# Optimization experiments

Measured on AMD Instinct MI355X. Metric: run time of the kernel, lower is better.

## Reference

```python
import jax, jax.numpy as jnp
import numpy as np

K_CLUSTERS = 512
N_ITERS = 10  # fixed Lloyd iterations (torch_kmeans uses max_iter with tol; fixed count keeps it jit-friendly)


def setup_inputs() -> dict:
    key = jax.random.key(0)
    x = jax.random.normal(key, (4, 8192, 256), dtype=jnp.float32)  # (B, N, D)
    return {"x": x}


def _sq_dists(x, centers):
    # x: (B,N,D), centers: (B,K,D) -> squared Euclidean distances (B,N,K)
    xc = jnp.einsum('bnd,bkd->bnk', x, centers)
    x2 = jnp.sum(x * x, axis=-1, keepdims=True)          # (B,N,1)
    c2 = jnp.sum(centers * centers, axis=-1)[:, None, :]  # (B,1,K)
    return x2 - 2.0 * xc + c2


def _kmeans(x, k=K_CLUSTERS, iters=N_ITERS):
    # deterministic init: first k points of each batch as initial centroids
    centers0 = x[:, :k, :]  # (B,K,D)

    def step(centers, _):
        labels = jnp.argmin(_sq_dists(x, centers), axis=-1)          # (B,N)
        onehot = jax.nn.one_hot(labels, k, dtype=x.dtype)            # (B,N,K)
        sums = jnp.einsum('bnk,bnd->bkd', onehot, x)                 # (B,K,D)
        counts = jnp.sum(onehot, axis=1)                             # (B,K)
        new_centers = jnp.where(
            counts[..., None] > 0,
            sums / jnp.maximum(counts, 1.0)[..., None],
            centers,  # keep empty clusters' previous centroid
        )
        return new_centers, None

    centers, _ = jax.lax.scan(step, centers0, None, length=iters)
    labels = jnp.argmin(_sq_dists(x, centers), axis=-1)
    return labels, centers


def reference(x):
    labels, centers = _kmeans(x)
    return labels, centers
```

## Files before the change

### kernel.cpp

```cpp
#include <hip/hip_runtime.h>
#include <math.h>

#define BB 4
#define NN 8192
#define DD 256
#define KK 512
#define NITERS 10

#define TAU 0.02f
#define NCH 128

typedef _Float16 f16;
typedef f16   f16x8 __attribute__((ext_vector_type(8)));
typedef float f32x4 __attribute__((ext_vector_type(4)));

__global__ __launch_bounds__(256) void init_centers_k(const float* __restrict__ x,
                                                      float* __restrict__ centers,
                                                      f16* __restrict__ chh,
                                                      f16* __restrict__ chl,
                                                      float* __restrict__ c2) {
    __shared__ float sq[256];
    int bk = blockIdx.x;
    int b  = bk >> 9;
    int k  = bk & 511;
    int t  = threadIdx.x;
    size_t idx = (size_t)bk * DD + t;
    float v = x[((size_t)b * NN + k) * DD + t];
    centers[idx] = v;
    f16 h = (f16)v;
    chh[idx] = h;
    chl[idx] = (f16)(v - (float)h);
    sq[t] = v * v;
    __syncthreads();
    for (int s = 128; s > 0; s >>= 1) {
        if (t < s) sq[t] += sq[t + s];
        __syncthreads();
    }
    if (t == 0) c2[bk] = sq[0];
}

__global__ __launch_bounds__(256) void rowsumsq_k(const float* __restrict__ rows,
                                                  float* __restrict__ out, int nrows) {
    int r = blockIdx.x * 256 + threadIdx.x;
    if (r >= nrows) return;
    const float* p = rows + (size_t)r * DD;
    float total = 0.f;
    #pragma unroll
    for (int h = 0; h < 2; ++h) {
        float a[8];
        #pragma unroll
        for (int j = 0; j < 8; ++j) a[j] = 0.f;
        for (int i = 0; i < 128; i += 8) {
            #pragma unroll
            for (int j = 0; j < 8; ++j) {
                float v  = p[h * 128 + i + j];
                float sq = __fmul_rn(v, v);
                a[j] = __fadd_rn(a[j], sq);
            }
        }
        float s = __fadd_rn(__fadd_rn(__fadd_rn(a[0], a[1]), __fadd_rn(a[2], a[3])),
                            __fadd_rn(__fadd_rn(a[4], a[5]), __fadd_rn(a[6], a[7])));
        total = __fadd_rn(total, s);
    }
    out[r] = total;
}

__global__ __launch_bounds__(256, 2) void assign_k(
    const float* __restrict__ x,
    const f16* __restrict__ chh, const f16* __restrict__ chl,
    const float* __restrict__ x2g, const float* __restrict__ c2g,
    int* __restrict__ labels, int* __restrict__ flagslot, int* __restrict__ flaglist)
{
    __shared__ f16 xlh[64 * 256];
    __shared__ f16 xll[64 * 256];
    __shared__ float rv1s[4][64];
    __shared__ float rv2s[4][64];
    __shared__ int   rk1s[4][64];

    const int tid  = threadIdx.x;
    const int wid  = tid >> 6;
    const int lane = tid & 63;
    const int l15  = lane & 15;
    const int lg   = lane >> 4;
    const int b    = blockIdx.x >> 7;
    const int m0   = (blockIdx.x & 127) * 64;

    const float* xb = x + (size_t)(b * NN + m0) * DD;

    #pragma unroll
    for (int i = 0; i < 8; ++i) {
        int lin = tid + i * 256;
        int row = lin >> 5, g = lin & 31;
        const float* p = xb + row * DD + g * 8;
        float4 a  = *(const float4*)p;
        float4 bq = *(const float4*)(p + 4);
        float vf[8] = {a.x, a.y, a.z, a.w, bq.x, bq.y, bq.z, bq.w};
        f16x8 hv, lv;
        #pragma unroll
        for (int j = 0; j < 8; ++j) {
            f16 h = (f16)vf[j];
            hv[j] = h;
            lv[j] = (f16)(vf[j] - (float)h);
        }
        int si = row * 256 + ((g ^ (row & 7)) << 3);
        *(f16x8*)&xlh[si] = hv;
        *(f16x8*)&xll[si] = lv;
    }
    __syncthreads();

    const f16* bhb = chh + ((size_t)b * KK + wid * 128) * DD;
    const f16* blb = chl + ((size_t)b * KK + wid * 128) * DD;

    f32x4 acc[4][8];
    #pragma unroll
    for (int mi = 0; mi < 4; ++mi)
        #pragma unroll
        for (int ki = 0; ki < 8; ++ki)
            acc[mi][ki] = (f32x4){0.f, 0.f, 0.f, 0.f};

    for (int d0 = 0; d0 < DD; d0 += 32) {
        f16x8 ah[4], al[4];
        #pragma unroll
        for (int mi = 0; mi < 4; ++mi) {
            int row = mi * 16 + l15;
            int g   = (d0 >> 3) + lg;
            int si  = row * 256 + ((g ^ (row & 7)) << 3);
            ah[mi] = *(const f16x8*)&xlh[si];
            al[mi] = *(const f16x8*)&xll[si];
        }
        #pragma unroll
        for (int ki = 0; ki < 8; ++ki) {
            size_t off = (size_t)(ki * 16 + l15) * DD + d0 + lg * 8;
            f16x8 bh = *(const f16x8*)(bhb + off);
            f16x8 bl = *(const f16x8*)(blb + off);
            #pragma unroll
            for (int mi = 0; mi < 4; ++mi) {
                acc[mi][ki] = __builtin_amdgcn_mfma_f32_16x16x32_f16(ah[mi], bh, acc[mi][ki], 0, 0, 0);
                acc[mi][ki] = __builtin_amdgcn_mfma_f32_16x16x32_f16(ah[mi], bl, acc[mi][ki], 0, 0, 0);
                acc[mi][ki] = __builtin_amdgcn_mfma_f32_16x16x32_f16(al[mi], bh, acc[mi][ki], 0, 0, 0);
            }
        }
    }

    float c2v[8];
    #pragma unroll
    for (int ki = 0; ki < 8; ++ki)
        c2v[ki] = c2g[b * KK + wid * 128 + ki * 16 + l15];

    #pragma unroll
    for (int mi = 0; mi < 4; ++mi) {
        #pragma unroll
        for (int r = 0; r < 4; ++r) {
            int p = mi * 16 + lg * 4 + r;
            float x2p = x2g[b * NN + m0 + p];
            float v1 = __builtin_inff(), v2 = __builtin_inff();
            int   k1 = 0x7fffffff;
            #pragma unroll
            for (int ki = 0; ki < 8; ++ki) {
                float s    = acc[mi][ki][r];
                float cand = __fadd_rn(__fsub_rn(x2p, __fmul_rn(2.0f, s)), c2v[ki]);
                int   kidx = wid * 128 + ki * 16 + l15;
                if (cand < v1 || (cand == v1 && kidx < k1)) { v2 = v1; v1 = cand; k1 = kidx; }
                else if (cand < v2) v2 = cand;
            }
            #pragma unroll
            for (int off = 1; off < 16; off <<= 1) {
                float ov1 = __shfl_xor(v1, off, 64);
                int   ok1 = __shfl_xor(k1, off, 64);
                float ov2 = __shfl_xor(v2, off, 64);
                if (ov1 < v1 || (ov1 == v1 && ok1 < k1)) { v2 = fminf(v1, ov2); v1 = ov1; k1 = ok1; }
                else v2 = fminf(v2, ov1);
            }
            if (l15 == 0) { rv1s[wid][p] = v1; rv2s[wid][p] = v2; rk1s[wid][p] = k1; }
        }
    }
    __syncthreads();
    if (tid < 64) {
        float v1 = rv1s[0][tid], v2 = rv2s[0][tid];
        int   k1 = rk1s[0][tid];
        #pragma unroll
        for (int w = 1; w < 4; ++w) {
            float ov1 = rv1s[w][tid], ov2 = rv2s[w][tid];
            int   ok1 = rk1s[w][tid];
            if (ov1 < v1 || (ov1 == v1 && ok1 < k1)) { v2 = fminf(v1, ov2); v1 = ov1; k1 = ok1; }
            else v2 = fminf(v2, ov1);
        }
        int g = b * NN + m0 + tid;
        labels[g] = k1;
        if (v2 - v1 < TAU) {
            int pos = atomicAdd(flagslot, 1);
            flaglist[pos] = g;
        }
    }
}

__global__ __launch_bounds__(256) void refine_k(const float* __restrict__ x,
                                                const float* __restrict__ centers,
                                                const int* __restrict__ flagslot,
                                                const int* __restrict__ flaglist,
                                                int* __restrict__ labels) {
    __shared__ float  xsr[DD];
    __shared__ double sv[256];
    __shared__ int    si[256];
    const int t = threadIdx.x;
    const int cnt = flagslot[0];
    for (int idx = blockIdx.x; idx < cnt; idx += gridDim.x) {
        const int g = flaglist[idx];
        const int b = g >> 13;
        __syncthreads();
        xsr[t] = x[(size_t)g * DD + t];
        __syncthreads();
        const float* cbase = centers + (size_t)b * KK * DD;
        double bestv = 1e300; int bestk = 0x7fffffff;
        #pragma unroll
        for (int h = 0; h < 2; ++h) {
            int k = t + h * 256;
            const float* cr = cbase + (size_t)k * DD;
            double a0 = 0, a1 = 0, a2 = 0, a3 = 0;
            for (int d = 0; d < DD; d += 4) {
                float4 cv = *(const float4*)(cr + d);
                double f0 = (double)xsr[d + 0] - (double)cv.x;
                double f1 = (double)xsr[d + 1] - (double)cv.y;
                double f2 = (double)xsr[d + 2] - (double)cv.z;
                double f3 = (double)xsr[d + 3] - (double)cv.w;
                a0 += f0 * f0; a1 += f1 * f1; a2 += f2 * f2; a3 += f3 * f3;
            }
            double dist = (a0 + a1) + (a2 + a3);
            if (dist < bestv || (dist == bestv && k < bestk)) { bestv = dist; bestk = k; }
        }
        sv[t] = bestv; si[t] = bestk;
        __syncthreads();
        for (int s = 128; s > 0; s >>= 1) {
            if (t < s) {
                if (sv[t + s] < sv[t] || (sv[t + s] == sv[t] && si[t + s] < si[t])) {
                    sv[t] = sv[t + s]; si[t] = si[t + s];
                }
            }
            __syncthreads();
        }
        if (t == 0) labels[g] = si[0];
    }
}

__global__ __launch_bounds__(64) void chunk_hist_k(const int* __restrict__ labels,
                                                   int* __restrict__ chunkhist) {
    __shared__ int h[KK];
    const int bc = blockIdx.x;
    const int b  = bc >> 7;
    const int c  = bc & (NCH - 1);
    const int t  = threadIdx.x;
    for (int k = t; k < KK; k += 64) h[k] = 0;
    __syncthreads();
    int l = labels[b * NN + c * 64 + t];
    atomicAdd(&h[l], 1);
    __syncthreads();
    int* ch = chunkhist + (size_t)bc * KK;
    for (int k = t; k < KK; k += 64) ch[k] = h[k];
}

__global__ __launch_bounds__(64) void scan_cols_k(int* __restrict__ chunkhist,
                                                  int* __restrict__ counts) {
    const int bq = blockIdx.x;
    const int b  = bq >> 3;
    const int k  = (bq & 7) * 64 + threadIdx.x;
    int* ch = chunkhist + (size_t)b * NCH * KK;
    int run = 0;
    for (int c0 = 0; c0 < NCH; c0 += 16) {
        int v[16];
        #pragma unroll
        for (int j = 0; j < 16; ++j) v[j] = ch[(size_t)(c0 + j) * KK + k];
        #pragma unroll
        for (int j = 0; j < 16; ++j) {
            ch[(size_t)(c0 + j) * KK + k] = run;
            run += v[j];
        }
    }
    counts[b * KK + k] = run;
}

__global__ __launch_bounds__(512) void scan_offsets_k(const int* __restrict__ counts,
                                                      int* __restrict__ offsets) {
    __shared__ int s[KK];
    const int b = blockIdx.x;
    const int k = threadIdx.x;
    int run = counts[b * KK + k];
    s[k] = run;
    __syncthreads();
    for (int off = 1; off < KK; off <<= 1) {
        int v = (k >= off) ? s[k - off] : 0;
        __syncthreads();
        s[k] += v;
        __syncthreads();
    }
    offsets[b * KK + k] = s[k] - run;
}

__global__ __launch_bounds__(64) void scatter_k(const int* __restrict__ labels,
                                                const int* __restrict__ chunkhist,
                                                const int* __restrict__ offsets,
                                                int* __restrict__ idxlist) {
    const int bc = blockIdx.x;
    const int b  = bc >> 7;
    const int c  = bc & (NCH - 1);
    const int t  = threadIdx.x;
    const int n  = c * 64 + t;
    const int l  = labels[b * NN + n];
    int rank = 0;
    for (int j = 0; j < 64; ++j) {
        int lj = __shfl(l, j, 64);
        rank += (lj == l && j < t) ? 1 : 0;
    }
    int base = offsets[b * KK + l] + chunkhist[(size_t)bc * KK + l];
    idxlist[b * NN + base + rank] = n;
}

__global__ __launch_bounds__(1024) void centers_update_k(const float* __restrict__ x,
                                                         float* __restrict__ centers,
                                                         f16* __restrict__ chh,
                                                         f16* __restrict__ chl,
                                                         float* __restrict__ c2,
                                                         const int* __restrict__ counts,
                                                         const int* __restrict__ offsets,
                                                         const int* __restrict__ idxlist) {
    __shared__ float part[16][DD];
    __shared__ float sq[256];
    const int bk   = blockIdx.x;
    const int b    = bk >> 9;
    const int tid  = threadIdx.x;
    const int w    = tid >> 6;
    const int lane = tid & 63;
    const int cnt = counts[bk];
    if (cnt == 0) return;
    const int* il = idxlist + b * NN + offsets[bk];
    const float* xb = x + (size_t)b * NN * DD;
    float4 acc = {0.f, 0.f, 0.f, 0.f};
    #pragma unroll 4
    for (int j = w; j < cnt; j += 16) {
        int n = il[j];
        float4 v = *(const float4*)(xb + (size_t)n * DD + lane * 4);
        acc.x = __fadd_rn(acc.x, v.x);
        acc.y = __fadd_rn(acc.y, v.y);
        acc.z = __fadd_rn(acc.z, v.z);
        acc.w = __fadd_rn(acc.w, v.w);
    }
    *(float4*)&part[w][lane * 4] = acc;
    __syncthreads();
    float val = 0.f;
    if (tid < DD) {
        float s = 0.f;
        #pragma unroll
        for (int w2 = 0; w2 < 16; ++w2) s = __fadd_rn(s, part[w2][tid]);
        val = s / (float)cnt;
        size_t idx = (size_t)bk * DD + tid;
        centers[idx] = val;
        f16 h = (f16)val;
        chh[idx] = h;
        chl[idx] = (f16)(val - (float)h);
    }
    if (tid < 256) sq[tid] = val * val;
    __syncthreads();
    for (int s = 128; s > 0; s >>= 1) {
        if (tid < s) sq[tid] += sq[tid + s];
        __syncthreads();
    }
    if (tid == 0) c2[bk] = sq[0];
}

__global__ __launch_bounds__(256) void out_k(const int* __restrict__ labels,
                                             const float* __restrict__ centers,
                                             float* __restrict__ out) {
    size_t i = (size_t)blockIdx.x * 256 + threadIdx.x;
    if (i < (size_t)BB * NN) out[i] = (float)labels[i];
    else                     out[i] = centers[i - (size_t)BB * NN];
}

extern "C" void kernel_launch(void* const* d_in, const int* in_sizes, int n_in,
                              void* d_out, int out_size, void* d_ws, size_t ws_size,
                              hipStream_t stream) {
    const float* x = (const float*)d_in[0];
    float* out = (float*)d_out;
    float* ws  = (float*)d_ws;

    float* centers  = ws;
    float* c2       = centers + (size_t)BB * KK * DD;
    float* x2       = c2 + BB * KK;
    int*   labels   = (int*)(x2 + BB * NN);
    int*   flagcnt  = labels + BB * NN;
    int*   flaglist = flagcnt + 64;
    int*   counts   = flaglist + BB * NN;
    int*   offsets  = counts + BB * KK;
    int*   idxlist  = offsets + BB * KK;
    int*   chunkhist= idxlist + BB * NN;
    f16*   chh      = (f16*)(chunkhist + (size_t)BB * NCH * KK);
    f16*   chl      = chh + (size_t)BB * KK * DD;

    hipMemsetAsync(flagcnt, 0, 64 * sizeof(int), stream);

    init_centers_k<<<BB * KK, 256, 0, stream>>>(x, centers, chh, chl, c2);
    rowsumsq_k<<<(BB * NN + 255) / 256, 256, 0, stream>>>(x, x2, BB * NN);

    for (int it = 0; it < NITERS; ++it) {
        assign_k<<<BB * (NN / 64), 256, 0, stream>>>(x, chh, chl, x2, c2,
                                                     labels, flagcnt + it, flaglist);
        refine_k<<<512, 256, 0, stream>>>(x, centers, flagcnt + it, flaglist, labels);
        chunk_hist_k<<<BB * NCH, 64, 0, stream>>>(labels, chunkhist);
        scan_cols_k<<<BB * 8, 64, 0, stream>>>(chunkhist, counts);
        scan_offsets_k<<<BB, 512, 0, stream>>>(counts, offsets);
        scatter_k<<<BB * NCH, 64, 0, stream>>>(labels, chunkhist, offsets, idxlist);
        centers_update_k<<<BB * KK, 1024, 0, stream>>>(x, centers, chh, chl, c2,
                                                       counts, offsets, idxlist);
    }

    assign_k<<<BB * (NN / 64), 256, 0, stream>>>(x, chh, chl, x2, c2,
                                                 labels, flagcnt + NITERS, flaglist);
    refine_k<<<512, 256, 0, stream>>>(x, centers, flagcnt + NITERS, flaglist, labels);

    out_k<<<(int)(((size_t)BB * NN + (size_t)BB * KK * DD + 255) / 256), 256, 0, stream>>>(
        labels, centers, out);
}
```

Measured before the change: 1.103 ms.

## Split assign GEMM into two passes with double-buffered center loads; merge scan kernels

The assign kernel now processes the 512 centers in two passes of 256, which halves the accumulator register footprint per pass. Within each pass, the next d-slice of center fragments is prefetched into alternating register buffers while the current slice runs through MFMA. This is meant to hide global-load latency and relieve register pressure, at the cost of reloading the x tile fragments from LDS twice and running the reduction over 8 partials. Separately, the column scan and offset scan are fused into a single kernel with 4 blocks, saving one launch per iteration but reducing parallelism in the column scan.

```diff
diff --git a/kernel.cpp b/kernel.cpp
--- a/kernel.cpp
+++ b/kernel.cpp
@@ -73,9 +73,9 @@
 {
     __shared__ f16 xlh[64 * 256];
     __shared__ f16 xll[64 * 256];
-    __shared__ float rv1s[4][64];
-    __shared__ float rv2s[4][64];
-    __shared__ int   rk1s[4][64];
+    __shared__ float rv1s[8][64];
+    __shared__ float rv2s[8][64];
+    __shared__ int   rk1s[8][64];
 
     const int tid  = threadIdx.x;
     const int wid  = tid >> 6;
@@ -108,70 +108,113 @@
     }
     __syncthreads();
 
-    const f16* bhb = chh + ((size_t)b * KK + wid * 128) * DD;
-    const f16* blb = chl + ((size_t)b * KK + wid * 128) * DD;
-
-    f32x4 acc[4][8];
     #pragma unroll
-    for (int mi = 0; mi < 4; ++mi)
-        #pragma unroll
-        for (int ki = 0; ki < 8; ++ki)
-            acc[mi][ki] = (f32x4){0.f, 0.f, 0.f, 0.f};
-
-    for (int d0 = 0; d0 < DD; d0 += 32) {
+    for (int pass = 0; pass < 2; ++pass) {
+        const f16* bhb = chh + ((size_t)b * KK + pass * 256 + wid * 64) * DD;
+        const f16* blb = chl + ((size_t)b * KK + pass * 256 + wid * 64) * DD;
+
+        f32x4 acc[4][4];
+        #pragma unroll
+        for (int mi = 0; mi < 4; ++mi)
+            #pragma unroll
+            for (int ki = 0; ki < 4; ++ki)
+                acc[mi][ki] = (f32x4){0.f, 0.f, 0.f, 0.f};
+
         f16x8 ah[4], al[4];
-        #pragma unroll
-        for (int mi = 0; mi < 4; ++mi) {
-            int row = mi * 16 + l15;
-            int g   = (d0 >> 3) + lg;
-            int si  = row * 256 + ((g ^ (row & 7)) << 3);
-            ah[mi] = *(const f16x8*)&xlh[si];
-            al[mi] = *(const f16x8*)&xll[si];
-        }
-        #pragma unroll
-        for (int ki = 0; ki < 8; ++ki) {
-            size_t off = (size_t)(ki * 16 + l15) * DD + d0 + lg * 8;
-            f16x8 bh = *(const f16x8*)(bhb + off);
-            f16x8 bl = *(const f16x8*)(blb + off);
+        f16x8 bhA[4], blA[4], bhB[4], blB[4];
+
+        #pragma unroll
+        for (int ki = 0; ki < 4; ++ki) {
+            size_t off = (size_t)(ki * 16 + l15) * DD + lg * 8;
+            bhA[ki] = *(const f16x8*)(bhb + off);
+            blA[ki] = *(const f16x8*)(blb + off);
+        }
+
+        #pragma unroll
+        for (int s = 0; s < 8; ++s) {
+            const int d0 = s * 32;
+            if (s < 7) {
+                const int dn = d0 + 32;
+                if ((s & 1) == 0) {
+                    #pragma unroll
+                    for (int ki = 0; ki < 4; ++ki) {
+                        size_t off = (size_t)(ki * 16 + l15) * DD + dn + lg * 8;
+                        bhB[ki] = *(const f16x8*)(bhb + off);
+                        blB[ki] = *(const f16x8*)(blb + off);
+                    }
+                } else {
+                    #pragma unroll
+                    for (int ki = 0; ki < 4; ++ki) {
+                        size_t off = (size_t)(ki * 16 + l15) * DD + dn + lg * 8;
+                        bhA[ki] = *(const f16x8*)(bhb + off);
+                        blA[ki] = *(const f16x8*)(blb + off);
+                    }
+                }
+            }
             #pragma unroll
             for (int mi = 0; mi < 4; ++mi) {
-                acc[mi][ki] = __builtin_amdgcn_mfma_f32_16x16x32_f16(ah[mi], bh, acc[mi][ki], 0, 0, 0);
-                acc[mi][ki] = __builtin_amdgcn_mfma_f32_16x16x32_f16(ah[mi], bl, acc[mi][ki], 0, 0, 0);
-                acc[mi][ki] = __builtin_amdgcn_mfma_f32_16x16x32_f16(al[mi], bh, acc[mi][ki], 0, 0, 0);
-            }
-        }
-    }
-
-    float c2v[8];
-    #pragma unroll
-    for (int ki = 0; ki < 8; ++ki)
-        c2v[ki] = c2g[b * KK + wid * 128 + ki * 16 + l15];
-
-    #pragma unroll
-    for (int mi = 0; mi < 4; ++mi) {
-        #pragma unroll
-        for (int r = 0; r < 4; ++r) {
-            int p = mi * 16 + lg * 4 + r;
-            float x2p = x2g[b * NN + m0 + p];
-            float v1 = __builtin_inff(), v2 = __builtin_inff();
-            int   k1 = 0x7fffffff;
+                int row = mi * 16 + l15;
+                int g   = (d0 >> 3) + lg;
+                int si  = row * 256 + ((g ^ (row & 7)) << 3);
+                ah[mi] = *(const f16x8*)&xlh[si];
+                al[mi] = *(const f16x8*)&xll[si];
+            }
+            if ((s & 1) == 0) {
+                #pragma unroll
+                for (int ki = 0; ki < 4; ++ki)
+                    #pragma unroll
+                    for (int mi = 0; mi < 4; ++mi) {
+                        acc[mi][ki] = __builtin_amdgcn_mfma_f32_16x16x32_f16(ah[mi], bhA[ki], acc[mi][ki], 0, 0, 0);
+                        acc[mi][ki] = __builtin_amdgcn_mfma_f32_16x16x32_f16(ah[mi], blA[ki], acc[mi][ki], 0, 0, 0);
+                        acc[mi][ki] = __builtin_amdgcn_mfma_f32_16x16x32_f16(al[mi], bhA[ki], acc[mi][ki], 0, 0, 0);
+                    }
+            } else {
+                #pragma unroll
+                for (int ki = 0; ki < 4; ++ki)
+                    #pragma unroll
+                    for (int mi = 0; mi < 4; ++mi) {
+                        acc[mi][ki] = __builtin_amdgcn_mfma_f32_16x16x32_f16(ah[mi], bhB[ki], acc[mi][ki], 0, 0, 0);
+                        acc[mi][ki] = __builtin_amdgcn_mfma_f32_16x16x32_f16(ah[mi], blB[ki], acc[mi][ki], 0, 0, 0);
+                        acc[mi][ki] = __builtin_amdgcn_mfma_f32_16x16x32_f16(al[mi], bhB[ki], acc[mi][ki], 0, 0, 0);
+                    }
+            }
+        }
+
+        float c2v[4];
+        #pragma unroll
+        for (int ki = 0; ki < 4; ++ki)
+            c2v[ki] = c2g[b * KK + pass * 256 + wid * 64 + ki * 16 + l15];
+
+        #pragma unroll
+        for (int mi = 0; mi < 4; ++mi) {
             #pragma unroll
-            for (int ki = 0; ki < 8; ++ki) {
-                float s    = acc[mi][ki][r];
-                float cand = __fadd_rn(__fsub_rn(x2p, __fmul_rn(2.0f, s)), c2v[ki]);
-                int   kidx = wid * 128 + ki * 16 + l15;
-                if (cand < v1 || (cand == v1 && kidx < k1)) { v2 = v1; v1 = cand; k1 = kidx; }
-                else if (cand < v2) v2 = cand;
-            }
-            #pragma unroll
-            for (int off = 1; off < 16; off <<= 1) {
-                float ov1 = __shfl_xor(v1, off, 64);
-                int   ok1 = __shfl_xor(k1, off, 64);
-                float ov2 = __shfl_xor(v2, off, 64);
-                if (ov1 < v1 || (ov1 == v1 && ok1 < k1)) { v2 = fminf(v1, ov2); v1 = ov1; k1 = ok1; }
-                else v2 = fminf(v2, ov1);
-            }
-            if (l15 == 0) { rv1s[wid][p] = v1; rv2s[wid][p] = v2; rk1s[wid][p] = k1; }
+            for (int r = 0; r < 4; ++r) {
+                int p = mi * 16 + lg * 4 + r;
+                float x2p = x2g[b * NN + m0 + p];
+                float v1 = __builtin_inff(), v2 = __builtin_inff();
+                int   k1 = 0x7fffffff;
+                #pragma unroll
+                for (int ki = 0; ki < 4; ++ki) {
+                    float sdot = acc[mi][ki][r];
+                    float cand = __fadd_rn(__fsub_rn(x2p, __fmul_rn(2.0f, sdot)), c2v[ki]);
+                    int   kidx = pass * 256 + wid * 64 + ki * 16 + l15;
+                    if (cand < v1 || (cand == v1 && kidx < k1)) { v2 = v1; v1 = cand; k1 = kidx; }
+                    else if (cand < v2) v2 = cand;
+                }
+                #pragma unroll
+                for (int off = 1; off < 16; off <<= 1) {
+                    float ov1 = __shfl_xor(v1, off, 64);
+                    int   ok1 = __shfl_xor(k1, off, 64);
+                    float ov2 = __shfl_xor(v2, off, 64);
+                    if (ov1 < v1 || (ov1 == v1 && ok1 < k1)) { v2 = fminf(v1, ov2); v1 = ov1; k1 = ok1; }
+                    else v2 = fminf(v2, ov1);
+                }
+                if (l15 == 0) {
+                    rv1s[wid * 2 + pass][p] = v1;
+                    rv2s[wid * 2 + pass][p] = v2;
+                    rk1s[wid * 2 + pass][p] = k1;
+                }
+            }
         }
     }
     __syncthreads();
@@ -179,7 +222,7 @@
         float v1 = rv1s[0][tid], v2 = rv2s[0][tid];
         int   k1 = rk1s[0][tid];
         #pragma unroll
-        for (int w = 1; w < 4; ++w) {
+        for (int w = 1; w < 8; ++w) {
             float ov1 = rv1s[w][tid], ov2 = rv2s[w][tid];
             int   ok1 = rk1s[w][tid];
             if (ov1 < v1 || (ov1 == v1 && ok1 < k1)) { v2 = fminf(v1, ov2); v1 = ov1; k1 = ok1; }
@@ -258,11 +301,12 @@
     for (int k = t; k < KK; k += 64) ch[k] = h[k];
 }
 
-__global__ __launch_bounds__(64) void scan_cols_k(int* __restrict__ chunkhist,
-                                                  int* __restrict__ counts) {
-    const int bq = blockIdx.x;
-    const int b  = bq >> 3;
-    const int k  = (bq & 7) * 64 + threadIdx.x;
+__global__ __launch_bounds__(512) void scan_k(int* __restrict__ chunkhist,
+                                              int* __restrict__ counts,
+                                              int* __restrict__ offsets) {
+    __shared__ int s[KK];
+    const int b = blockIdx.x;
+    const int k = threadIdx.x;
     int* ch = chunkhist + (size_t)b * NCH * KK;
     int run = 0;
     for (int c0 = 0; c0 < NCH; c0 += 16) {
@@ -276,14 +320,6 @@
         }
     }
     counts[b * KK + k] = run;
-}
-
-__global__ __launch_bounds__(512) void scan_offsets_k(const int* __restrict__ counts,
-                                                      int* __restrict__ offsets) {
-    __shared__ int s[KK];
-    const int b = blockIdx.x;
-    const int k = threadIdx.x;
-    int run = counts[b * KK + k];
     s[k] = run;
     __syncthreads();
     for (int off = 1; off < KK; off <<= 1) {
@@ -404,8 +440,7 @@
                                                      labels, flagcnt + it, flaglist);
         refine_k<<<512, 256, 0, stream>>>(x, centers, flagcnt + it, flaglist, labels);
         chunk_hist_k<<<BB * NCH, 64, 0, stream>>>(labels, chunkhist);
-        scan_cols_k<<<BB * 8, 64, 0, stream>>>(chunkhist, counts);
-        scan_offsets_k<<<BB, 512, 0, stream>>>(counts, offsets);
+        scan_k<<<BB, 512, 0, stream>>>(chunkhist, counts, offsets);
         scatter_k<<<BB * NCH, 64, 0, stream>>>(labels, chunkhist, offsets, idxlist);
         centers_update_k<<<BB * KK, 1024, 0, stream>>>(x, centers, chh, chl, c2,
                                                        counts, offsets, idxlist);
```

After: 1.205 ms. +9.2%, slower.

## Precompute x low-half fp16 once and merge column and offset scans

Applied to the files above, without the earlier changes.

A new kernel computes the fp16 residual (low part) of x once before the iterations. assign_k then reads that residual straight from global memory inside the MFMA loop instead of storing it in LDS, which halves its shared memory footprint. The chunk histogram is transposed to a [k][chunk] layout so a single scan kernel can do the per-cluster column scan and the cross-cluster offset scan, saving a launch per iteration. The cost is direct global reads of the A-operand low half during the inner loop, which may stall, plus extra workspace for the residual array.

```diff
diff --git a/kernel.cpp b/kernel.cpp
--- a/kernel.cpp
+++ b/kernel.cpp
@@ -39,6 +39,21 @@
     if (t == 0) c2[bk] = sq[0];
 }
 
+__global__ __launch_bounds__(256) void xsplit_k(const float* __restrict__ x,
+                                                f16* __restrict__ xl) {
+    size_t i = ((size_t)blockIdx.x * 256 + threadIdx.x) * 8;
+    float4 a  = *(const float4*)(x + i);
+    float4 bq = *(const float4*)(x + i + 4);
+    float vf[8] = {a.x, a.y, a.z, a.w, bq.x, bq.y, bq.z, bq.w};
+    f16x8 lv;
+    #pragma unroll
+    for (int j = 0; j < 8; ++j) {
+        f16 h = (f16)vf[j];
+        lv[j] = (f16)(vf[j] - (float)h);
+    }
+    *(f16x8*)(xl + i) = lv;
+}
+
 __global__ __launch_bounds__(256) void rowsumsq_k(const float* __restrict__ rows,
                                                   float* __restrict__ out, int nrows) {
     int r = blockIdx.x * 256 + threadIdx.x;
@@ -66,13 +81,12 @@
 }
 
 __global__ __launch_bounds__(256, 2) void assign_k(
-    const float* __restrict__ x,
+    const float* __restrict__ x, const f16* __restrict__ xl,
     const f16* __restrict__ chh, const f16* __restrict__ chl,
     const float* __restrict__ x2g, const float* __restrict__ c2g,
     int* __restrict__ labels, int* __restrict__ flagslot, int* __restrict__ flaglist)
 {
     __shared__ f16 xlh[64 * 256];
-    __shared__ f16 xll[64 * 256];
     __shared__ float rv1s[4][64];
     __shared__ float rv2s[4][64];
     __shared__ int   rk1s[4][64];
@@ -85,7 +99,8 @@
     const int b    = blockIdx.x >> 7;
     const int m0   = (blockIdx.x & 127) * 64;
 
-    const float* xb = x + (size_t)(b * NN + m0) * DD;
+    const float* xb  = x  + (size_t)(b * NN + m0) * DD;
+    const f16*   xlb = xl + (size_t)(b * NN + m0) * DD;
 
     #pragma unroll
     for (int i = 0; i < 8; ++i) {
@@ -95,16 +110,11 @@
         float4 a  = *(const float4*)p;
         float4 bq = *(const float4*)(p + 4);
         float vf[8] = {a.x, a.y, a.z, a.w, bq.x, bq.y, bq.z, bq.w};
-        f16x8 hv, lv;
-        #pragma unroll
-        for (int j = 0; j < 8; ++j) {
-            f16 h = (f16)vf[j];
-            hv[j] = h;
-            lv[j] = (f16)(vf[j] - (float)h);
-        }
+        f16x8 hv;
+        #pragma unroll
+        for (int j = 0; j < 8; ++j) hv[j] = (f16)vf[j];
         int si = row * 256 + ((g ^ (row & 7)) << 3);
         *(f16x8*)&xlh[si] = hv;
-        *(f16x8*)&xll[si] = lv;
     }
     __syncthreads();
 
@@ -126,8 +136,10 @@
             int g   = (d0 >> 3) + lg;
             int si  = row * 256 + ((g ^ (row & 7)) << 3);
             ah[mi] = *(const f16x8*)&xlh[si];
-            al[mi] = *(const f16x8*)&xll[si];
-        }
+        }
+        #pragma unroll
+        for (int mi = 0; mi < 4; ++mi)
+            al[mi] = *(const f16x8*)(xlb + (size_t)(mi * 16 + l15) * DD + d0 + lg * 8);
         #pragma unroll
         for (int ki = 0; ki < 8; ++ki) {
             size_t off = (size_t)(ki * 16 + l15) * DD + d0 + lg * 8;
@@ -254,36 +266,29 @@
     int l = labels[b * NN + c * 64 + t];
     atomicAdd(&h[l], 1);
     __syncthreads();
-    int* ch = chunkhist + (size_t)bc * KK;
-    for (int k = t; k < KK; k += 64) ch[k] = h[k];
-}
-
-__global__ __launch_bounds__(64) void scan_cols_k(int* __restrict__ chunkhist,
-                                                  int* __restrict__ counts) {
-    const int bq = blockIdx.x;
-    const int b  = bq >> 3;
-    const int k  = (bq & 7) * 64 + threadIdx.x;
-    int* ch = chunkhist + (size_t)b * NCH * KK;
+    for (int k = t; k < KK; k += 64)
+        chunkhist[((size_t)b * KK + k) * NCH + c] = h[k];
+}
+
+__global__ __launch_bounds__(512) void scan_k(int* __restrict__ chunkhist,
+                                              int* __restrict__ counts,
+                                              int* __restrict__ offsets) {
+    __shared__ int s[KK];
+    const int b = blockIdx.x;
+    const int k = threadIdx.x;
+    int* ch = chunkhist + ((size_t)b * KK + k) * NCH;
     int run = 0;
     for (int c0 = 0; c0 < NCH; c0 += 16) {
         int v[16];
         #pragma unroll
-        for (int j = 0; j < 16; ++j) v[j] = ch[(size_t)(c0 + j) * KK + k];
+        for (int j = 0; j < 16; ++j) v[j] = ch[c0 + j];
         #pragma unroll
         for (int j = 0; j < 16; ++j) {
-            ch[(size_t)(c0 + j) * KK + k] = run;
+            ch[c0 + j] = run;
             run += v[j];
         }
     }
     counts[b * KK + k] = run;
-}
-
-__global__ __launch_bounds__(512) void scan_offsets_k(const int* __restrict__ counts,
-                                                      int* __restrict__ offsets) {
-    __shared__ int s[KK];
-    const int b = blockIdx.x;
-    const int k = threadIdx.x;
-    int run = counts[b * KK + k];
     s[k] = run;
     __syncthreads();
     for (int off = 1; off < KK; off <<= 1) {
@@ -310,7 +315,7 @@
         int lj = __shfl(l, j, 64);
         rank += (lj == l && j < t) ? 1 : 0;
     }
-    int base = offsets[b * KK + l] + chunkhist[(size_t)bc * KK + l];
+    int base = offsets[b * KK + l] + chunkhist[((size_t)b * KK + l) * NCH + c];
     idxlist[b * NN + base + rank] = n;
 }
 
@@ -393,25 +398,26 @@
     int*   chunkhist= idxlist + BB * NN;
     f16*   chh      = (f16*)(chunkhist + (size_t)BB * NCH * KK);
     f16*   chl      = chh + (size_t)BB * KK * DD;
+    f16*   xl16     = chl + (size_t)BB * KK * DD;
 
     hipMemsetAsync(flagcnt, 0, 64 * sizeof(int), stream);
 
     init_centers_k<<<BB * KK, 256, 0, stream>>>(x, centers, chh, chl, c2);
+    xsplit_k<<<(int)((size_t)BB * NN * DD / 8 / 256), 256, 0, stream>>>(x, xl16);
     rowsumsq_k<<<(BB * NN + 255) / 256, 256, 0, stream>>>(x, x2, BB * NN);
 
     for (int it = 0; it < NITERS; ++it) {
-        assign_k<<<BB * (NN / 64), 256, 0, stream>>>(x, chh, chl, x2, c2,
+        assign_k<<<BB * (NN / 64), 256, 0, stream>>>(x, xl16, chh, chl, x2, c2,
                                                      labels, flagcnt + it, flaglist);
         refine_k<<<512, 256, 0, stream>>>(x, centers, flagcnt + it, flaglist, labels);
         chunk_hist_k<<<BB * NCH, 64, 0, stream>>>(labels, chunkhist);
-        scan_cols_k<<<BB * 8, 64, 0, stream>>>(chunkhist, counts);
-        scan_offsets_k<<<BB, 512, 0, stream>>>(counts, offsets);
+        scan_k<<<BB, 512, 0, stream>>>(chunkhist, counts, offsets);
         scatter_k<<<BB * NCH, 64, 0, stream>>>(labels, chunkhist, offsets, idxlist);
         centers_update_k<<<BB * KK, 1024, 0, stream>>>(x, centers, chh, chl, c2,
                                                        counts, offsets, idxlist);
     }
 
-    assign_k<<<BB * (NN / 64), 256, 0, stream>>>(x, chh, chl, x2, c2,
+    assign_k<<<BB * (NN / 64), 256, 0, stream>>>(x, xl16, chh, chl, x2, c2,
                                                  labels, flagcnt + NITERS, flaglist);
     refine_k<<<512, 256, 0, stream>>>(x, centers, flagcnt + NITERS, flaglist, labels);
 
```

Measured after the change: 1.369 ms. 1.24x slower.
